# Kernel optimization log

Hardware: AMD Instinct MI355X
Metric: run time of the kernel (lower is better)

## Reference

```python
import jax, jax.numpy as jnp
import numpy as np

BN_EPS = 1e-5


def cond_conv(x, att_w, att_b, weight, pad):
    """CondConv: per-sample expert-mixed conv.
    x: [N,C,H,W]; att_w: [K,C]; att_b: [K]; weight: [K,O,I,kh,kw]; pad: (ph,pw)."""
    pooled = x.mean(axis=(2, 3))                         # [N,C]  (AdaptiveAvgPool2d(1))
    att = jax.nn.sigmoid(pooled @ att_w.T + att_b)       # [N,K]  (1x1 conv + sigmoid)
    agg_w = jnp.einsum('nk,koihw->noihw', att, weight)   # per-sample kernels [N,O,I,kh,kw]

    def conv1(xi, wi):
        return jax.lax.conv_general_dilated(
            xi[None], wi, window_strides=(1, 1),
            padding=[(pad[0], pad[0]), (pad[1], pad[1])],
            dimension_numbers=('NCHW', 'OIHW', 'NCHW'))[0]

    return jax.vmap(conv1)(x, agg_w)                     # [N,O,H,W]


def batchnorm(x, gamma, beta):
    # training-mode BN: biased batch stats over (N,H,W)
    mean = x.mean(axis=(0, 2, 3), keepdims=True)
    var = x.var(axis=(0, 2, 3), keepdims=True)
    xn = (x - mean) * jax.lax.rsqrt(var + BN_EPS)
    return xn * gamma[None, :, None, None] + beta[None, :, None, None]


def channel_shuffle(x, g):
    N, C, H, W = x.shape
    return x.reshape(N, g, C // g, H, W).transpose(0, 2, 1, 3, 4).reshape(N, C, H, W)


def setup_inputs() -> dict:
    key = jax.random.key(0)
    ks = jax.random.split(key, 8)
    N, C, H, W = 32, 256, 64, 64
    Cb, K = C // 4, 4
    inp = {
        'x': jax.random.normal(ks[0], (N, C, H, W), jnp.float32),
        'sq_att_w': jax.random.normal(ks[1], (K, Cb), jnp.float32) * 0.1,
        'sq_att_b': jnp.zeros((K,), jnp.float32),
        'sq_w': jax.random.normal(ks[2], (K, Cb, Cb, 3, 3), jnp.float32) * 0.05,
        'sq_g': jnp.ones((Cb,), jnp.float32),
        'sq_b': jnp.zeros((Cb,), jnp.float32),
        'ver_att_w': jax.random.normal(ks[3], (K, Cb), jnp.float32) * 0.1,
        'ver_att_b': jnp.zeros((K,), jnp.float32),
        'ver_w': jax.random.normal(ks[4], (K, Cb, Cb, 3, 1), jnp.float32) * 0.05,
        'ver_g': jnp.ones((Cb,), jnp.float32),
        'ver_b': jnp.zeros((Cb,), jnp.float32),
        'hor_att_w': jax.random.normal(ks[5], (K, Cb), jnp.float32) * 0.1,
        'hor_att_b': jnp.zeros((K,), jnp.float32),
        'hor_w': jax.random.normal(ks[6], (K, Cb, Cb, 1, 3), jnp.float32) * 0.05,
        'hor_g': jnp.ones((Cb,), jnp.float32),
        'hor_b': jnp.zeros((Cb,), jnp.float32),
    }
    return inp


def reference(x, sq_att_w, sq_att_b, sq_w, sq_g, sq_b,
              ver_att_w, ver_att_b, ver_w, ver_g, ver_b,
              hor_att_w, hor_att_b, hor_w, hor_g, hor_b):
    # q_Split: chunk into 4 along channels
    s0, s1, s2, s3 = jnp.split(x, 4, axis=1)
    # square branch: CondConv 3x3 pad 1 + BN
    sq = batchnorm(cond_conv(s1, sq_att_w, sq_att_b, sq_w, (1, 1)), sq_g, sq_b)
    # vertical branch: CondConv 3x1 pad (1,0) + BN (crop layer is Identity since offset=0)
    ve = batchnorm(cond_conv(s2, ver_att_w, ver_att_b, ver_w, (1, 0)), ver_g, ver_b)
    # horizontal branch: CondConv 1x3 pad (0,1) + BN
    ho = batchnorm(cond_conv(s3, hor_att_w, hor_att_b, hor_w, (0, 1)), hor_g, hor_b)
    out = jnp.concatenate((s0, sq, ve, ho), axis=1)
    return channel_shuffle(out, 8)
```

## Files before the change

kernel.cpp:

```cpp
#include <hip/hip_runtime.h>
#include <cstddef>
#include <cstdint>


typedef __attribute__((ext_vector_type(8))) short frag8;
typedef __attribute__((ext_vector_type(16))) float accf16;

#define HW 4096
#define CNT_INV (1.0f / 131072.0f)
#define CSTR 1056
#define RSTR 8448
#define XT_BR (32ull * 66 * 8448)

#define WS_POOLED 0
#define WS_SS     24576
#define WS_PST    24960
#define WS_WBF_SQ  221568
#define WS_WBF_VER 811392
#define WS_WBF_HOR 1008000
#define WS_XT      1204608
#define WS_CVOUT   14586240

__device__ __forceinline__ int shuf_ch(int c) { return ((c & 31) << 3) | (c >> 5); }

__device__ __forceinline__ unsigned bf16pair(float a, float b) {
    unsigned ua = __builtin_bit_cast(unsigned, a);
    unsigned ub = __builtin_bit_cast(unsigned, b);
    ua = (ua + 0x7fffu + ((ua >> 16) & 1u)) >> 16;
    ub = (ub + 0x7fffu + ((ub >> 16) & 1u)) >> 16;
    return ua | (ub << 16);
}

__device__ __forceinline__ unsigned short bf16r(float a) {
    unsigned ua = __builtin_bit_cast(unsigned, a);
    return (unsigned short)((ua + 0x7fffu + ((ua >> 16) & 1u)) >> 16);
}

__device__ __forceinline__ float bf16lo(unsigned u) {
    return __builtin_bit_cast(float, u << 16);
}
__device__ __forceinline__ float bf16hi(unsigned u) {
    return __builtin_bit_cast(float, u & 0xffff0000u);
}

__device__ __forceinline__ void gload_lds16(const void* g, void* l) {
    __builtin_amdgcn_global_load_lds(
        (const __attribute__((address_space(1))) void*)g,
        (__attribute__((address_space(3))) void*)l, 16, 0, 0);
}

__global__ void __launch_bounds__(256) prepass_kernel(
    const float* __restrict__ x, unsigned char* __restrict__ xt,
    float* __restrict__ pooled4) {
    const int bid = blockIdx.x;
    const int hq = bid & 3;
    const int c8 = (bid >> 2) & 7;
    const int n = (bid >> 5) & 31;
    const int b = bid >> 10;
    const int tid = threadIdx.x;
    const int w = tid & 63, q = tid >> 6;
    const float* xb = x + (size_t)(n * 256 + 64 * (b + 1) + c8 * 8) * HW;
    unsigned char* xtb = xt + (size_t)b * XT_BR + (size_t)n * 66 * RSTR + c8 * CSTR;

    float ps[8] = {0.f, 0.f, 0.f, 0.f, 0.f, 0.f, 0.f, 0.f};
#pragma unroll
    for (int it = 0; it < 4; ++it) {
        const int h = hq * 16 + it * 4 + q;
        float v[8];
#pragma unroll
        for (int j = 0; j < 8; ++j) v[j] = xb[(size_t)j * HW + h * 64 + w];
        unsigned pkk[4];
#pragma unroll
        for (int j = 0; j < 4; ++j) pkk[j] = bf16pair(v[2 * j], v[2 * j + 1]);
        *(uint4*)(xtb + (size_t)(h + 1) * RSTR + (w + 1) * 16) = *(uint4*)pkk;
#pragma unroll
        for (int j = 0; j < 8; ++j) ps[j] += v[j];
    }
    if (hq == 0) {
        for (int idx = tid; idx < 260; idx += 256) {
            int p, slot;
            if (idx < 66)       { p = 0;         slot = idx; }
            else if (idx < 132) { p = 65;        slot = idx - 66; }
            else if (idx < 196) { p = idx - 131; slot = 0; }
            else                { p = idx - 195; slot = 65; }
            *(uint4*)(xtb + (size_t)p * RSTR + slot * 16) = uint4{0, 0, 0, 0};
        }
    }
    __shared__ float red[4][8];
#pragma unroll
    for (int j = 0; j < 8; ++j)
#pragma unroll
        for (int off = 32; off; off >>= 1) ps[j] += __shfl_down(ps[j], off, 64);
    if ((tid & 63) == 0)
#pragma unroll
        for (int j = 0; j < 8; ++j) red[q][j] = ps[j];
    __syncthreads();
    if (tid < 8)
        pooled4[hq * 6144 + (b * 32 + n) * 64 + c8 * 8 + tid] =
            red[0][tid] + red[1][tid] + red[2][tid] + red[3][tid];
}

template <int TAPS>
__device__ __forceinline__ void aggbf_body(const float* __restrict__ w,
                                           const float* __restrict__ pooled_b,
                                           const float* __restrict__ aw,
                                           const float* __restrict__ ab,
                                           unsigned* __restrict__ wbf, int bid) {
    const int tid = threadIdx.x;
    int idx = bid * 256 + tid;
    int ip = idx & 31;
    int o  = (idx >> 5) & 63;
    int t  = (idx >> 11) % TAPS;
    int n  = (idx >> 11) / TAPS;

    __shared__ float satt[4];
    if (tid < 64) {
        const int base = n * 64 + tid;
        float p = (pooled_b[base] + pooled_b[base + 6144] +
                   pooled_b[base + 12288] + pooled_b[base + 18432]) *
                  (1.f / 4096.f);
#pragma unroll
        for (int k = 0; k < 4; ++k) {
            float v = p * aw[k * 64 + tid];
#pragma unroll
            for (int off = 32; off; off >>= 1) v += __shfl_down(v, off, 64);
            if (tid == 0) satt[k] = 1.f / (1.f + expf(-(v + ab[k])));
        }
    }
    __syncthreads();
    const float a0 = satt[0], a1 = satt[1], a2 = satt[2], a3 = satt[3];

    constexpr int PS = 64 * 64 * TAPS;
    int base = (o * 64 + ip * 2) * TAPS + t;
    float v0 = a0*w[base] + a1*w[PS+base] + a2*w[2*PS+base] + a3*w[3*PS+base];
    int base1 = base + TAPS;
    float v1 = a0*w[base1] + a1*w[PS+base1] + a2*w[2*PS+base1] + a3*w[3*PS+base1];
    int f = ip >> 2, jj = ip & 3;
    wbf[(((n * TAPS + t) * 8 + f) * 64 + o) * 4 + jj] = bf16pair(v0, v1);
}

__global__ void __launch_bounds__(256) aggbf_all_kernel(
    const float* __restrict__ pooled,
    const float* __restrict__ aw0, const float* __restrict__ ab0,
    const float* __restrict__ aw1, const float* __restrict__ ab1,
    const float* __restrict__ aw2, const float* __restrict__ ab2,
    const float* __restrict__ sq_w, const float* __restrict__ ver_w,
    const float* __restrict__ hor_w,
    unsigned* __restrict__ wsq, unsigned* __restrict__ wver,
    unsigned* __restrict__ whor) {
    int bid = blockIdx.x;
    if (bid < 2304)
        aggbf_body<9>(sq_w, pooled, aw0, ab0, wsq, bid);
    else if (bid < 3072)
        aggbf_body<3>(ver_w, pooled + 2048, aw1, ab1, wver, bid - 2304);
    else
        aggbf_body<3>(hor_w, pooled + 4096, aw2, ab2, whor, bid - 3072);
}

#define LOADA(dst, tt) \
    _Pragma("unroll") for (int kk = 0; kk < 4; ++kk) { \
        dst[kk]     = wp[(tt) * 512 + kk * 128]; \
        dst[4 + kk] = wp[(tt) * 512 + kk * 128 + 32]; \
    }

#define TAPSTEP(tt, CUR) { \
    const int r_ = (tt) / KW, dw_ = (tt) % KW - PW; \
    const unsigned char* bp_ = xs + (rh * 2 + r_) * RSTR + hi * CSTR + \
                               (wcol + dw_ + 1) * 16; \
    _Pragma("unroll") for (int kk = 0; kk < 4; ++kk) { \
        frag8 b0 = *(const frag8*)(bp_ + kk * 2 * CSTR); \
        frag8 b1 = *(const frag8*)(bp_ + kk * 2 * CSTR + RSTR); \
        a00 = __builtin_amdgcn_mfma_f32_32x32x16_bf16(CUR[kk],     b0, a00, 0, 0, 0); \
        a10 = __builtin_amdgcn_mfma_f32_32x32x16_bf16(CUR[4 + kk], b0, a10, 0, 0, 0); \
        a01 = __builtin_amdgcn_mfma_f32_32x32x16_bf16(CUR[kk],     b1, a01, 0, 0, 0); \
        a11 = __builtin_amdgcn_mfma_f32_32x32x16_bf16(CUR[4 + kk], b1, a11, 0, 0, 0); \
    } }

template <int KH, int KW, int PH, int PW>
__device__ __forceinline__ void conv_body(
    const unsigned char* __restrict__ xt, const unsigned* __restrict__ wbf,
    unsigned short* __restrict__ cvout, float* __restrict__ pst, int cbase,
    int bid, unsigned char* xs, float (*red1)[2][2][16],
    float (*red2)[2][2][16]) {
    constexpr int TAPS = KH * KW;
    constexpr int HB = 4;
    constexpr int ROWS = HB + KH - 1;
    constexpr int NCH = (ROWS * RSTR + 1023) >> 10;
    const int hb = bid & 15, n = bid >> 4;
    const int h0 = hb * HB;
    const int tid = threadIdx.x;
    const int lane = tid & 63, wv = tid >> 6;
    const int rh = wv >> 1, wn = wv & 1;
    const int l31 = lane & 31, hi = lane >> 5;
    const int wcol = wn * 32 + l31;

    {
        const unsigned char* src = xt +
            (size_t)(n * 66 + h0 + (KH == 1 ? 1 : 0)) * RSTR + lane * 16;
#pragma unroll
        for (int c = wv; c < NCH; c += 4)
            gload_lds16(src + (c << 10), xs + (c << 10));
    }

    const frag8* wp = (const frag8*)wbf + (size_t)n * TAPS * 512 + hi * 64 + l31;
    frag8 aA[8], aB[8];
    LOADA(aA, 0);
    __syncthreads();

    accf16 a00 = {}, a01 = {}, a10 = {}, a11 = {};
#pragma unroll
    for (int t = 0; t < TAPS; t += 2) {
        if (t + 1 < TAPS) LOADA(aB, t + 1);
        TAPSTEP(t, aA);
        if (t + 2 < TAPS) LOADA(aA, t + 2);
        if (t + 1 < TAPS) TAPSTEP(t + 1, aB);
    }

#pragma unroll
    for (int rg = 0; rg < 16; ++rg) {
        float u1 = a00[rg] + a01[rg];
        float u2 = a00[rg] * a00[rg] + a01[rg] * a01[rg];
        float w1 = a10[rg] + a11[rg];
        float w2 = a10[rg] * a10[rg] + a11[rg] * a11[rg];
#pragma unroll
        for (int off = 16; off; off >>= 1) {
            u1 += __shfl_down(u1, off, 32);
            u2 += __shfl_down(u2, off, 32);
            w1 += __shfl_down(w1, off, 32);
            w2 += __shfl_down(w2, off, 32);
        }
        if (l31 == 0) {
            red1[wv][0][hi][rg] = u1; red2[wv][0][hi][rg] = u2;
            red1[wv][1][hi][rg] = w1; red2[wv][1][hi][rg] = w2;
        }
    }
    __syncthreads();

    {
        unsigned short* xo = (unsigned short*)xs;
        const int r0 = rh * 2;
#pragma unroll
        for (int rg = 0; rg < 16; ++rg) {
            const int o = (rg & 3) + 8 * (rg >> 2) + 4 * hi;
            xo[o * 256 + r0 * 64 + wcol]            = bf16r(a00[rg]);
            xo[o * 256 + (r0 + 1) * 64 + wcol]      = bf16r(a01[rg]);
            xo[(o + 32) * 256 + r0 * 64 + wcol]     = bf16r(a10[rg]);
            xo[(o + 32) * 256 + (r0 + 1) * 64 + wcol] = bf16r(a11[rg]);
        }
    }
    if (tid < 64) {
        const int rg = tid & 15, hi2 = (tid >> 4) & 1, wm2 = tid >> 5;
        float s1 = 0.f, s2 = 0.f;
#pragma unroll
        for (int v = 0; v < 4; ++v) {
            s1 += red1[v][wm2][hi2][rg];
            s2 += red2[v][wm2][hi2][rg];
        }
        const int o = wm2 * 32 + (rg & 3) + 8 * (rg >> 2) + 4 * hi2;
        const int slot = n * 16 + hb;
        pst[o * 1024 + slot] = s1;
        pst[o * 1024 + 512 + slot] = s2;
    }
    __syncthreads();

    {
        const unsigned short* xo = (const unsigned short*)xs;
        const int ch8 = tid >> 5, in32 = tid & 31;
#pragma unroll
        for (int it = 0; it < 8; ++it) {
            const int ch = it * 8 + ch8;
            uint4 v = *(const uint4*)(xo + ch * 256 + in32 * 8);
            *(uint4*)((unsigned char*)cvout +
                      (size_t)(n * 192 + (cbase - 64) + ch) * 8192 +
                      h0 * 128 + in32 * 16) = v;
        }
    }
}

__device__ __forceinline__ void s0_body(const float* __restrict__ x,
                                        float* __restrict__ out, int sid) {
    const int c8 = sid & 7, n = sid >> 3, tid = threadIdx.x;
#pragma unroll
    for (int j = 0; j < 8; ++j) {
        const int c = c8 * 8 + j;
        const float4* s = (const float4*)(x + (size_t)(n * 256 + c) * HW);
        float4* d = (float4*)(out + (size_t)(n * 256 + shuf_ch(c)) * HW);
#pragma unroll
        for (int it = 0; it < 4; ++it) d[tid + it * 256] = s[tid + it * 256];
    }
}

__global__ void __launch_bounds__(256, 3) conv_all_kernel(
    const float* __restrict__ x, const unsigned char* __restrict__ xt,
    const unsigned* __restrict__ wsq, const unsigned* __restrict__ wver,
    const unsigned* __restrict__ whor,
    unsigned short* __restrict__ cvout, float* __restrict__ pst,
    float* __restrict__ out) {
    __shared__ __align__(16) unsigned char xs[6 * RSTR + 512];
    __shared__ float red1[4][2][2][16], red2[4][2][2][16];
    int raw = blockIdx.x;
    if (raw >= 1536) { s0_body(x, out, raw - 1536); return; }
    int bid = (raw & 7) * 192 + (raw >> 3);
    if (bid < 512)
        conv_body<3, 3, 1, 1>(xt, wsq, cvout, pst, 64, bid, xs, red1, red2);
    else if (bid < 1024)
        conv_body<3, 1, 1, 0>(xt + XT_BR, wver, cvout, pst + 65536, 128,
                              bid - 512, xs, red1, red2);
    else
        conv_body<1, 3, 0, 1>(xt + 2 * XT_BR, whor, cvout, pst + 131072, 192,
                              bid - 1024, xs, red1, red2);
}

__global__ void __launch_bounds__(256) bnstats_all_kernel(
    const float* __restrict__ pst,
    const float* __restrict__ g0, const float* __restrict__ b0,
    const float* __restrict__ g1, const float* __restrict__ b1,
    const float* __restrict__ g2, const float* __restrict__ b2,
    float* __restrict__ ss) {
    int br = blockIdx.x >> 6, o = blockIdx.x & 63, t = threadIdx.x;
    const float* gamma = (br == 0) ? g0 : (br == 1) ? g1 : g2;
    const float* beta  = (br == 0) ? b0 : (br == 1) ? b1 : b2;
    const float* p = pst + br * 65536 + o * 1024;
    float s1 = 0.f, s2 = 0.f;
    for (int i = t; i < 512; i += 256) {
        s1 += p[i];
        s2 += p[512 + i];
    }
#pragma unroll
    for (int off = 32; off; off >>= 1) {
        s1 += __shfl_down(s1, off, 64);
        s2 += __shfl_down(s2, off, 64);
    }
    __shared__ float r1[4], r2[4];
    if ((t & 63) == 0) { r1[t >> 6] = s1; r2[t >> 6] = s2; }
    __syncthreads();
    if (t == 0) {
        float S1 = r1[0] + r1[1] + r1[2] + r1[3];
        float S2 = r2[0] + r2[1] + r2[2] + r2[3];
        float mean = S1 * CNT_INV;
        float var = S2 * CNT_INV - mean * mean;
        float scale = rsqrtf(var + 1e-5f) * gamma[o];
        ss[br * 128 + o * 2 + 0] = scale;
        ss[br * 128 + o * 2 + 1] = beta[o] - mean * scale;
    }
}

__global__ void __launch_bounds__(256) bn_all_kernel(
    const unsigned short* __restrict__ cvout, float* __restrict__ out,
    const float* __restrict__ ss) {
    int g = blockIdx.x;
    int half = g & 1;
    int n = (g >> 1) & 31;
    int o = (g >> 6) & 63;
    int sub = g >> 12;
    float scale = ss[sub * 128 + o * 2], shift = ss[sub * 128 + o * 2 + 1];
    const uint4* src = (const uint4*)(cvout +
        (size_t)(n * 192 + sub * 64 + o) * HW + half * 2048) + threadIdx.x;
    float* dst = out + (size_t)(n * 256 + shuf_ch(64 * (sub + 1) + o)) * HW +
                 half * 2048 + threadIdx.x * 8;
    uint4 r = *src;
    float4 f0, f1;
    f0.x = fmaf(bf16lo(r.x), scale, shift);
    f0.y = fmaf(bf16hi(r.x), scale, shift);
    f0.z = fmaf(bf16lo(r.y), scale, shift);
    f0.w = fmaf(bf16hi(r.y), scale, shift);
    f1.x = fmaf(bf16lo(r.z), scale, shift);
    f1.y = fmaf(bf16hi(r.z), scale, shift);
    f1.z = fmaf(bf16lo(r.w), scale, shift);
    f1.w = fmaf(bf16hi(r.w), scale, shift);
    *(float4*)dst = f0;
    *(float4*)(dst + 4) = f1;
}

extern "C" void kernel_launch(void* const* d_in, const int* in_sizes, int n_in,
                              void* d_out, int out_size, void* d_ws, size_t ws_size,
                              hipStream_t stream) {
    const float* x        = (const float*)d_in[0];
    const float* sq_att_w = (const float*)d_in[1];
    const float* sq_att_b = (const float*)d_in[2];
    const float* sq_w     = (const float*)d_in[3];
    const float* sq_g     = (const float*)d_in[4];
    const float* sq_b     = (const float*)d_in[5];
    const float* ver_att_w= (const float*)d_in[6];
    const float* ver_att_b= (const float*)d_in[7];
    const float* ver_w    = (const float*)d_in[8];
    const float* ver_g    = (const float*)d_in[9];
    const float* ver_b    = (const float*)d_in[10];
    const float* hor_att_w= (const float*)d_in[11];
    const float* hor_att_b= (const float*)d_in[12];
    const float* hor_w    = (const float*)d_in[13];
    const float* hor_g    = (const float*)d_in[14];
    const float* hor_b    = (const float*)d_in[15];
    float* out = (float*)d_out;
    float* ws = (float*)d_ws;

    float* pooled = ws + WS_POOLED;
    float* ss     = ws + WS_SS;
    float* pst    = ws + WS_PST;
    unsigned* wbf_sq  = (unsigned*)(ws + WS_WBF_SQ);
    unsigned* wbf_ver = (unsigned*)(ws + WS_WBF_VER);
    unsigned* wbf_hor = (unsigned*)(ws + WS_WBF_HOR);
    unsigned char* xt = (unsigned char*)(ws + WS_XT);
    unsigned short* cvout = (unsigned short*)(ws + WS_CVOUT);

    prepass_kernel<<<3072, 256, 0, stream>>>(x, xt, pooled);
    aggbf_all_kernel<<<3840, 256, 0, stream>>>(pooled,
                                               sq_att_w, sq_att_b,
                                               ver_att_w, ver_att_b,
                                               hor_att_w, hor_att_b,
                                               sq_w, ver_w, hor_w,
                                               wbf_sq, wbf_ver, wbf_hor);
    conv_all_kernel<<<1792, 256, 0, stream>>>(x, xt, wbf_sq, wbf_ver, wbf_hor,
                                              cvout, pst, out);
    bnstats_all_kernel<<<192, 256, 0, stream>>>(pst, sq_g, sq_b, ver_g, ver_b,
                                                hor_g, hor_b, ss);
    bn_all_kernel<<<12288, 256, 0, stream>>>(cvout, out, ss);
}
```

Baseline: 146.7 us.

## Process two conv tiles per block and spread s0 copy across conv blocks

The conv kernel now launches 768 blocks, each running two consecutive conv tiles of the same branch with a barrier between them, instead of one tile per block. The separate s0 passthrough blocks are dropped; every block copies up to three shuffled s0 channels after its conv work. The aim is to cut block launch and scheduling overhead, and to overlap the memory-bound copy with conv blocks rather than leaving it as a tail wave. In exchange, each block does a longer serial run of work, and the smaller grid may not fill all compute units evenly.

```diff
diff --git a/kernel.cpp b/kernel.cpp
--- a/kernel.cpp
+++ b/kernel.cpp
@@ -242,9 +242,9 @@
 #pragma unroll
         for (int rg = 0; rg < 16; ++rg) {
             const int o = (rg & 3) + 8 * (rg >> 2) + 4 * hi;
-            xo[o * 256 + r0 * 64 + wcol]            = bf16r(a00[rg]);
-            xo[o * 256 + (r0 + 1) * 64 + wcol]      = bf16r(a01[rg]);
-            xo[(o + 32) * 256 + r0 * 64 + wcol]     = bf16r(a10[rg]);
+            xo[o * 256 + r0 * 64 + wcol]              = bf16r(a00[rg]);
+            xo[o * 256 + (r0 + 1) * 64 + wcol]        = bf16r(a01[rg]);
+            xo[(o + 32) * 256 + r0 * 64 + wcol]       = bf16r(a10[rg]);
             xo[(o + 32) * 256 + (r0 + 1) * 64 + wcol] = bf16r(a11[rg]);
         }
     }
@@ -274,19 +274,6 @@
                       (size_t)(n * 192 + (cbase - 64) + ch) * 8192 +
                       h0 * 128 + in32 * 16) = v;
         }
-    }
-}
-
-__device__ __forceinline__ void s0_body(const float* __restrict__ x,
-                                        float* __restrict__ out, int sid) {
-    const int c8 = sid & 7, n = sid >> 3, tid = threadIdx.x;
-#pragma unroll
-    for (int j = 0; j < 8; ++j) {
-        const int c = c8 * 8 + j;
-        const float4* s = (const float4*)(x + (size_t)(n * 256 + c) * HW);
-        float4* d = (float4*)(out + (size_t)(n * 256 + shuf_ch(c)) * HW);
-#pragma unroll
-        for (int it = 0; it < 4; ++it) d[tid + it * 256] = s[tid + it * 256];
     }
 }
 
@@ -298,17 +285,41 @@
     float* __restrict__ out) {
     __shared__ __align__(16) unsigned char xs[6 * RSTR + 512];
     __shared__ float red1[4][2][2][16], red2[4][2][2][16];
-    int raw = blockIdx.x;
-    if (raw >= 1536) { s0_body(x, out, raw - 1536); return; }
-    int bid = (raw & 7) * 192 + (raw >> 3);
-    if (bid < 512)
-        conv_body<3, 3, 1, 1>(xt, wsq, cvout, pst, 64, bid, xs, red1, red2);
-    else if (bid < 1024)
-        conv_body<3, 1, 1, 0>(xt + XT_BR, wver, cvout, pst + 65536, 128,
-                              bid - 512, xs, red1, red2);
-    else
-        conv_body<1, 3, 0, 1>(xt + 2 * XT_BR, whor, cvout, pst + 131072, 192,
-                              bid - 1024, xs, red1, red2);
+    const int raw = blockIdx.x;
+    const int bid = (raw & 7) * 96 + (raw >> 3);
+    const int br = bid >> 8;
+    const int b = bid & 255;
+
+#pragma unroll
+    for (int j = 0; j < 2; ++j) {
+        const int tile = b * 2 + j;
+        if (j) __syncthreads();
+        if (br == 0)
+            conv_body<3, 3, 1, 1>(xt, wsq, cvout, pst, 64, tile,
+                                  xs, red1, red2);
+        else if (br == 1)
+            conv_body<3, 1, 1, 0>(xt + XT_BR, wver, cvout, pst + 65536, 128,
+                                  tile, xs, red1, red2);
+        else
+            conv_body<1, 3, 0, 1>(xt + 2 * XT_BR, whor, cvout,
+                                  pst + 131072, 192, tile, xs, red1, red2);
+    }
+
+    {
+        const int tid = threadIdx.x;
+#pragma unroll
+        for (int j = 0; j < 3; ++j) {
+            const int id = raw * 3 + j;
+            if (id < 2048) {
+                const int n = id >> 6, c = id & 63;
+                const float4* s = (const float4*)(x + (size_t)(n * 256 + c) * HW);
+                float4* d = (float4*)(out + (size_t)(n * 256 + shuf_ch(c)) * HW);
+#pragma unroll
+                for (int it = 0; it < 4; ++it)
+                    d[tid + it * 256] = s[tid + it * 256];
+            }
+        }
+    }
 }
 
 __global__ void __launch_bounds__(256) bnstats_all_kernel(
@@ -410,8 +421,8 @@
                                                hor_att_w, hor_att_b,
                                                sq_w, ver_w, hor_w,
                                                wbf_sq, wbf_ver, wbf_hor);
-    conv_all_kernel<<<1792, 256, 0, stream>>>(x, xt, wbf_sq, wbf_ver, wbf_hor,
-                                              cvout, pst, out);
+    conv_all_kernel<<<768, 256, 0, stream>>>(x, xt, wbf_sq, wbf_ver, wbf_hor,
+                                             cvout, pst, out);
     bnstats_all_kernel<<<192, 256, 0, stream>>>(pst, sq_g, sq_b, ver_g, ver_b,
                                                 hor_g, hor_b, ss);
     bn_all_kernel<<<12288, 256, 0, stream>>>(cvout, out, ss);
```

Measured after the change: 203.7 us. 1.39x slower.
